# Kernel optimization log

Measured on AMD Instinct MI355X. Metric: run time of the kernel, lower is better.

The kernel has to match this reference:

```python
import jax, jax.numpy as jnp
import numpy as np

B, T, NX = 2, 2048, 512
H = 2                    # n_head (structurally forced to 2 by rns() broadcasting)
L = 64                   # num landmarks (cfg.MODEL.LANDMARK)
K = 32                   # rns neighbors per token
HD = NX // H // 2        # differential head dim = 128
EPS = 1e-5


def setup_inputs() -> dict:
    key = jax.random.key(0)
    ks = jax.random.split(key, 16)
    inp = {}
    inp["x"] = jax.random.normal(ks[0], (B, T, NX), jnp.float32)
    # linear weights (torch nn.Linear stores [out,in], applies x @ W.T)
    inp["wq"] = jax.random.normal(ks[1], (NX, NX), jnp.float32) * 0.02
    inp["wk"] = jax.random.normal(ks[2], (NX, NX), jnp.float32) * 0.02
    inp["wv"] = jax.random.normal(ks[3], (NX, NX), jnp.float32) * 0.02
    inp["wo"] = jax.random.normal(ks[4], (NX, NX), jnp.float32) * 0.02
    # landmark modulation params (kaiming-normal-ish init)
    inp["m1"] = jax.random.normal(ks[5], (2 * H, L, 1), jnp.float32)
    inp["m2"] = jax.random.normal(ks[6], (2 * H, 1, L), jnp.float32)
    # differential-attention lambda params
    inp["lq1"] = jax.random.normal(ks[7], (HD,), jnp.float32) * 0.1
    inp["lk1"] = jax.random.normal(ks[8], (HD,), jnp.float32) * 0.1
    inp["lq2"] = jax.random.normal(ks[9], (HD,), jnp.float32) * 0.1
    inp["lk2"] = jax.random.normal(ks[10], (HD,), jnp.float32) * 0.1
    inp["rms_g"] = jnp.ones((2 * HD,), jnp.float32)
    inp["l"] = 3  # layer depth for lambda_init_fn
    inp["num_landmark"] = L
    inp["rns_indices"] = jax.random.randint(ks[11], (B, T, K), 0, T)
    # random.sample(range(t), L) -> distinct indices
    inp["landmark"] = jax.random.permutation(ks[12], T)[:L]
    return inp


def _forward(x, wq, wk, wv, wo, m1, m2, lq1, lk1, lq2, lk2, rms_g,
             l, rns_indices, landmark):
    b, t, nx = x.shape
    hd = nx // H // 2
    q = x @ wq.T
    k = x @ wk.T
    v = x @ wv.T
    qh = q.reshape(b, t, 2 * H, hd).transpose(0, 2, 1, 3)   # [b,2H,t,hd]
    kh = k.reshape(b, t, 2 * H, hd).transpose(0, 2, 3, 1)   # [b,2H,hd,t]
    vh = v.reshape(b, t, H, 2 * hd).transpose(0, 2, 1, 3)   # [b,H,t,2hd]

    # landmark (Nystrom) low-rank factors, L2-normalized over head dim
    sq = qh[:, :, landmark, :]                               # [b,2H,L,hd]
    sk = kh[:, :, :, landmark]                               # [b,2H,hd,L]
    sq = sq / jnp.linalg.norm(sq, axis=3, keepdims=True)
    sk = sk / jnp.linalg.norm(sk, axis=2, keepdims=True)
    sq = m1[None] * sq
    sk = m2[None] * sk

    w1 = jnp.matmul(qh, sk)                                  # [b,2H,t,L]
    w2 = jnp.matmul(sq, kh)                                  # [b,2H,L,t]
    w = jnp.matmul(w1, w2)                                   # [b,2H,t,t]

    lam_init = 0.8 - 0.6 * np.exp(-0.3 * l)
    lam = jnp.exp(jnp.sum(lq1 * lk1)) - jnp.exp(jnp.sum(lq2 * lk2)) + lam_init

    # rns symmetric sparse mask: mask[b,i,j]=1 iff j in rns_indices[b,i] AND i in rns_indices[b,j]
    bi = jnp.arange(b)[:, None, None]
    ti = jnp.arange(t)[None, :, None]
    m = jnp.zeros((b, t, t), x.dtype).at[bi, ti, rns_indices].set(1.0)
    m = m * m.transpose(0, 2, 1)
    m4 = m[:, None]                                          # broadcast over heads

    p = jax.nn.softmax(w * m4 - 1e9 * (1.0 - m4), axis=-1)   # [b,2H,t,t]
    p5 = p.reshape(b, H, 2, t, t)
    # differential mixing (note: second term indexes the HEAD dim, requires H==2)
    wmix = (p5[:, :, 0] - lam * p5[:, :, 1]) + ((1.0 - lam) * p5[:, 1] - p5[:, 0])
    a = jnp.matmul(wmix, vh)                                 # [b,H,t,2hd]

    # RMSNorm sub-layer + (1 - lambda_init) scaling
    a = a * jax.lax.rsqrt(jnp.mean(a * a, axis=-1, keepdims=True) + EPS) * rms_g
    a = a * (1.0 - lam_init)
    return a.transpose(0, 2, 1, 3).reshape(b, t, H * 2 * hd) @ wo.T


def reference(x, wq, wk, wv, wo, m1, m2, lq1, lk1, lq2, lk2, rms_g,
              l, num_landmark, rns_indices, landmark):
    return _forward(x, wq, wk, wv, wo, m1, m2, lq1, lk1, lq2, lk2, rms_g,
                    l, rns_indices, landmark)
```

## Files before the change

kernel.cpp:

```cpp
#include <hip/hip_runtime.h>
#include <hip/hip_bf16.h>

#define BB 2
#define TT 2048
#define NX 512
#define NH 4
#define HD 128
#define LL 64
#define KK 32

typedef __bf16 bf16x8 __attribute__((ext_vector_type(8)));
typedef float f32x4 __attribute__((ext_vector_type(4)));
typedef unsigned short us;
typedef const unsigned int __attribute__((address_space(1)))* gptr_t;
typedef unsigned int __attribute__((address_space(3)))* lptr_t;

__device__ __forceinline__ us f2bf(float f) {
    unsigned u = __float_as_uint(f);
    unsigned r = (u + 0x7fffu + ((u >> 16) & 1u)) >> 16;
    return (us)r;
}
__device__ __forceinline__ float bf2f(us h) {
    return __uint_as_float(((unsigned)h) << 16);
}

__global__ void k_split_all(const float* __restrict__ x,
                            const float* __restrict__ wq, const float* __restrict__ wk,
                            const float* __restrict__ wv, const float* __restrict__ wo,
                            us* __restrict__ x_hi, us* __restrict__ x_lo,
                            us* __restrict__ wqkv_hi, us* __restrict__ wqkv_lo,
                            us* __restrict__ wo_hi, us* __restrict__ wo_lo,
                            const float* __restrict__ lq1, const float* __restrict__ lk1,
                            const float* __restrict__ lq2, const float* __restrict__ lk2,
                            const int* __restrict__ lint, float* __restrict__ scal)
{
    const int bidx = blockIdx.x;
    if (bidx == 3072) {
        const int tid = threadIdx.x;
        if (tid < 64) {
            float s1 = lq1[tid] * lk1[tid] + lq1[tid + 64] * lk1[tid + 64];
            float s2 = lq2[tid] * lk2[tid] + lq2[tid + 64] * lk2[tid + 64];
            for (int off = 32; off; off >>= 1) { s1 += __shfl_xor(s1, off); s2 += __shfl_xor(s2, off); }
            if (tid == 0) {
                float lam_init = 0.8f - 0.6f * expf(-0.3f * (float)lint[0]);
                scal[0] = expf(s1) - expf(s2) + lam_init;
                scal[1] = lam_init;
            }
        }
        return;
    }
    const float* src;
    us* hi;
    us* lo;
    int pos;
    if (bidx < 2048) {
        src = x; hi = x_hi; lo = x_lo;
        pos = bidx * 1024 + threadIdx.x * 4;
    } else {
        const int w = (bidx - 2048) >> 8;
        const int p = (bidx - 2048) & 255;
        pos = p * 1024 + threadIdx.x * 4;
        if (w == 0)      { src = wq; hi = wqkv_hi;          lo = wqkv_lo; }
        else if (w == 1) { src = wk; hi = wqkv_hi + 262144; lo = wqkv_lo + 262144; }
        else if (w == 2) { src = wv; hi = wqkv_hi + 524288; lo = wqkv_lo + 524288; }
        else             { src = wo; hi = wo_hi;            lo = wo_lo; }
    }
    const float4 v = *reinterpret_cast<const float4*>(src + pos);
    ushort4 h, l;
    h.x = f2bf(v.x); l.x = f2bf(v.x - bf2f(h.x));
    h.y = f2bf(v.y); l.y = f2bf(v.y - bf2f(h.y));
    h.z = f2bf(v.z); l.z = f2bf(v.z - bf2f(h.z));
    h.w = f2bf(v.w); l.w = f2bf(v.w - bf2f(h.w));
    *reinterpret_cast<ushort4*>(hi + pos) = h;
    *reinterpret_cast<ushort4*>(lo + pos) = l;
}

template<int BN, int MODE>
__global__ __launch_bounds__(256) void k_gemm_big(
    const us* __restrict__ a_hi, const us* __restrict__ a_lo,
    const us* __restrict__ b_hi, const us* __restrict__ b_lo,
    float* __restrict__ c2, float* __restrict__ cout,
    us* __restrict__ qs_hi, us* __restrict__ qs_lo,
    us* __restrict__ ks_hi, us* __restrict__ ks_lo)
{
    constexpr int NB = BN / 32;
    constexpr int NSTEP = (MODE == 0 ? 24 : 16);
    __shared__ us lsA[64 * 64];
    __shared__ us lsB[BN * 64];
    const int tid = threadIdx.x;
    const int m0 = blockIdx.x * 64, n0 = blockIdx.y * BN;
    const int region = n0 >> 9;
    const int ncol0 = n0 & 511;
    const int l = tid & 63, wid = tid >> 6;
    const int wr = (wid >> 1) * 32, wc = (wid & 1) * (BN / 2);
    const int lr = l & 15;
    const int lkb = (l >> 4) * 16;
    f32x4 acc[2][NB] = {};

    const int r8 = tid >> 3;
    const int swzc8 = (((tid & 7) ^ (r8 & 7)) * 8);

    for (int kt = 0; kt < NSTEP; ++kt) {
        const int seg = kt >> 3;
        const int koff = (kt & 7) * 64;
        const us* ab;
        const us* bb;
        if constexpr (MODE == 0) {
            ab = (seg < 2 ? a_hi : a_lo) + koff + swzc8;
            bb = (seg == 1 ? b_lo : b_hi) + koff + swzc8;
        } else {
            ab = (seg == 0 ? a_hi : a_lo) + koff + swzc8;
            bb = b_hi + koff + swzc8;
        }
        #pragma unroll
        for (int j = 0; j < 2; ++j)
            __builtin_amdgcn_global_load_lds((gptr_t)(ab + (size_t)(m0 + j * 32 + r8) * 512),
                                             (lptr_t)(lsA + j * 2048 + tid * 8), 16, 0, 0);
        #pragma unroll
        for (int j = 0; j < BN / 32; ++j)
            __builtin_amdgcn_global_load_lds((gptr_t)(bb + (size_t)(n0 + j * 32 + r8) * 512),
                                             (lptr_t)(lsB + j * 2048 + tid * 8), 16, 0, 0);
        __syncthreads();
        bf16x8 af[2][2], bfr[NB][2];
        #pragma unroll
        for (int m = 0; m < 2; ++m) {
            const int row = wr + m * 16 + lr;
            #pragma unroll
            for (int kk = 0; kk < 2; ++kk) {
                const int cb = (kk * 64 + lkb) ^ ((row & 7) << 4);
                af[m][kk] = *reinterpret_cast<const bf16x8*>(
                    (const char*)lsA + row * 128 + cb);
            }
        }
        #pragma unroll
        for (int n = 0; n < NB; ++n) {
            const int row = wc + n * 16 + lr;
            #pragma unroll
            for (int kk = 0; kk < 2; ++kk) {
                const int cb = (kk * 64 + lkb) ^ ((row & 7) << 4);
                bfr[n][kk] = *reinterpret_cast<const bf16x8*>(
                    (const char*)lsB + row * 128 + cb);
            }
        }
        #pragma unroll
        for (int kk = 0; kk < 2; ++kk)
            #pragma unroll
            for (int m = 0; m < 2; ++m)
                #pragma unroll
                for (int n = 0; n < NB; ++n)
                    acc[m][n] = __builtin_amdgcn_mfma_f32_16x16x32_bf16(
                        af[m][kk], bfr[n][kk], acc[m][n], 0, 0, 0);
        __syncthreads();
    }

    if constexpr (MODE == 0) {
        if (region < 2) {
            us* sh = (region == 0) ? qs_hi : ks_hi;
            us* slo = (region == 0) ? qs_lo : ks_lo;
            #pragma unroll
            for (int m = 0; m < 2; ++m) {
                const int row = m0 + wr + m * 16 + (l >> 4) * 4;
                #pragma unroll
                for (int n = 0; n < NB; ++n) {
                    const int col = ncol0 + wc + n * 16 + lr;
                    #pragma unroll
                    for (int r = 0; r < 4; ++r) {
                        const float val = acc[m][n][r];
                        const us h = f2bf(val);
                        sh[(size_t)(row + r) * 512 + col] = h;
                        slo[(size_t)(row + r) * 512 + col] = f2bf(val - bf2f(h));
                    }
                }
            }
        } else {
            #pragma unroll
            for (int m = 0; m < 2; ++m) {
                const int row = m0 + wr + m * 16 + (l >> 4) * 4;
                #pragma unroll
                for (int n = 0; n < NB; ++n) {
                    const int col = ncol0 + wc + n * 16 + lr;
                    #pragma unroll
                    for (int r = 0; r < 4; ++r)
                        c2[(size_t)(row + r) * 512 + col] = acc[m][n][r];
                }
            }
        }
    } else {
        #pragma unroll
        for (int m = 0; m < 2; ++m) {
            const int row = m0 + wr + m * 16 + (l >> 4) * 4;
            #pragma unroll
            for (int n = 0; n < NB; ++n) {
                const int col = n0 + wc + n * 16 + lr;
                #pragma unroll
                for (int r = 0; r < 4; ++r)
                    cout[(size_t)(row + r) * 512 + col] = acc[m][n][r];
            }
        }
    }
}

__global__ __launch_bounds__(256) void k_gemm_w12(
    const us* __restrict__ q_hi, const us* __restrict__ q_lo,
    const us* __restrict__ k_hi, const us* __restrict__ k_lo,
    const us* __restrict__ kn_hi, const us* __restrict__ kn_lo,
    const us* __restrict__ qn_hi, const us* __restrict__ qn_lo,
    float* __restrict__ w1, float* __restrict__ w2t)
{
    __shared__ us lsA[64 * 32];
    __shared__ us lsB[64 * 32];
    const int tid = threadIdx.x;
    const int m0 = blockIdx.x * 64;
    const int bh = blockIdx.y;
    const int h = bh & 3, b = bh >> 2;
    const int z = blockIdx.z;
    const us* ah = (z ? k_hi : q_hi) + ((size_t)b * 2048) * 512 + h * 128;
    const us* al = (z ? k_lo : q_lo) + ((size_t)b * 2048) * 512 + h * 128;
    const us* bh_p = (z ? qn_hi : kn_hi) + (size_t)bh * 64 * 128;
    const us* bl_p = (z ? qn_lo : kn_lo) + (size_t)bh * 64 * 128;
    float* C = (z ? w2t : w1) + (size_t)bh * 2048 * 64;

    const int l = tid & 63, wid = tid >> 6;
    const int wr = (wid >> 1) * 32, wc = (wid & 1) * 32;
    const int lr = l & 15, lk8 = (l >> 4) * 8;
    f32x4 acc[2][2] = {};
    const int srow = tid >> 2, scol = (tid & 3) * 8;

    for (int kt = 0; kt < 12; ++kt) {
        const int seg = kt >> 2;
        const int koff = (kt & 3) * 32;
        const us* ab = (seg < 2 ? ah : al) + koff + scol;
        const us* bb = (seg == 1 ? bl_p : bh_p) + koff + scol;
        __builtin_amdgcn_global_load_lds((gptr_t)(ab + (size_t)(m0 + srow) * 512),
                                         (lptr_t)(lsA + tid * 8), 16, 0, 0);
        __builtin_amdgcn_global_load_lds((gptr_t)(bb + (size_t)srow * 128),
                                         (lptr_t)(lsB + tid * 8), 16, 0, 0);
        __syncthreads();
        bf16x8 af[2], bfr[2];
        #pragma unroll
        for (int m = 0; m < 2; ++m)
            af[m] = *reinterpret_cast<const bf16x8*>(&lsA[(wr + m * 16 + lr) * 32 + lk8]);
        #pragma unroll
        for (int n = 0; n < 2; ++n)
            bfr[n] = *reinterpret_cast<const bf16x8*>(&lsB[(wc + n * 16 + lr) * 32 + lk8]);
        #pragma unroll
        for (int m = 0; m < 2; ++m)
            #pragma unroll
            for (int n = 0; n < 2; ++n)
                acc[m][n] = __builtin_amdgcn_mfma_f32_16x16x32_bf16(af[m], bfr[n], acc[m][n], 0, 0, 0);
        __syncthreads();
    }

    #pragma unroll
    for (int m = 0; m < 2; ++m) {
        const int row = m0 + wr + m * 16 + (l >> 4) * 4;
        #pragma unroll
        for (int n = 0; n < 2; ++n) {
            const int col = wc + n * 16 + lr;
            #pragma unroll
            for (int r = 0; r < 4; ++r)
                C[(size_t)(row + r) * 64 + col] = acc[m][n][r];
        }
    }
}

__global__ void k_norm_lm(const us* __restrict__ q_hi, const us* __restrict__ q_lo,
                          const us* __restrict__ k_hi, const us* __restrict__ k_lo,
                          const float* __restrict__ m1, const float* __restrict__ m2,
                          const int* __restrict__ landmark,
                          us* __restrict__ qn_hi, us* __restrict__ qn_lo,
                          us* __restrict__ kn_hi, us* __restrict__ kn_lo)
{
    const int idx = blockIdx.x;
    const int l = idx & 63;
    const int h = (idx >> 6) & 3;
    const int b = idx >> 8;
    const int lm = landmark[l];
    const int d = threadIdx.x;

    const size_t qoff = ((size_t)(b * TT + lm)) * NX + h * HD;
    const float qa = bf2f(q_hi[qoff + d]) + bf2f(q_lo[qoff + d]);
    const float qb = bf2f(q_hi[qoff + d + 64]) + bf2f(q_lo[qoff + d + 64]);
    const float ka = bf2f(k_hi[qoff + d]) + bf2f(k_lo[qoff + d]);
    const float kb = bf2f(k_hi[qoff + d + 64]) + bf2f(k_lo[qoff + d + 64]);
    float sq = qa * qa + qb * qb;
    float sk = ka * ka + kb * kb;
    for (int off = 32; off; off >>= 1) { sq += __shfl_xor(sq, off); sk += __shfl_xor(sk, off); }
    const float invq = rsqrtf(sq) * m1[h * LL + l];
    const float invk = rsqrtf(sk) * m2[h * LL + l];
    const size_t base = (((size_t)(b * NH + h)) * LL + l) * HD;
    const float vq0 = qa * invq, vq1 = qb * invq;
    const float vk0 = ka * invk, vk1 = kb * invk;
    us h0;
    h0 = f2bf(vq0); qn_hi[base + d] = h0;      qn_lo[base + d] = f2bf(vq0 - bf2f(h0));
    h0 = f2bf(vq1); qn_hi[base + d + 64] = h0; qn_lo[base + d + 64] = f2bf(vq1 - bf2f(h0));
    h0 = f2bf(vk0); kn_hi[base + d] = h0;      kn_lo[base + d] = f2bf(vk0 - bf2f(h0));
    h0 = f2bf(vk1); kn_hi[base + d + 64] = h0; kn_lo[base + d + 64] = f2bf(vk1 - bf2f(h0));
}

__global__ void k_colsum(const float* __restrict__ v, float* __restrict__ cs)
{
    const int e = blockIdx.x * 256 + threadIdx.x;
    const int b = e >> 9, c = e & 511;
    const int t0 = blockIdx.y * 128;
    const float* p = v + ((size_t)b) * TT * NX + c;
    float s = 0.f;
    for (int t = t0; t < t0 + 128; ++t) s += p[(size_t)t * NX];
    atomicAdd(&cs[e], s);
}

__global__ __launch_bounds__(256) void k_sparse_attn(
    const float* __restrict__ w1, const float* __restrict__ w2t,
    const float* __restrict__ v, const float* __restrict__ cs,
    const int* __restrict__ rns, const float* __restrict__ rms_g,
    const float* __restrict__ scal,
    us* __restrict__ ao_hi, us* __restrict__ ao_lo)
{
    const int wid = threadIdx.x >> 6;
    const int lane = threadIdx.x & 63;
    const int bi = blockIdx.x * 4 + wid;
    const int b = bi >> 11, i = bi & 2047;

    __shared__ int   sl[4][32];
    __shared__ float plog[4][96];
    __shared__ float wmm[4][2][32];
    __shared__ float w1s[4][3][64];

    const int myidx = lane & 31;
    const int cand = rns[(size_t)bi * KK + myidx];
    int dup = 0;
    #pragma unroll
    for (int kk = 0; kk < 31; ++kk) {
        const int other = __shfl(cand, kk);
        dup |= (kk < myidx) & (other == cand);
    }
    const int* jrow = rns + ((size_t)(b * TT + cand)) * KK + (lane >> 5) * 16;
    int found = 0;
    #pragma unroll
    for (int kk = 0; kk < 16; ++kk) found |= (jrow[kk] == i);
    found |= __shfl_xor(found, 32);
    const int keep = (!dup) && found;
    const unsigned long long mask = __ballot(keep) & 0xffffffffull;
    const int sc = __popcll(mask);
    const int pos = __popcll(mask & ((1ull << myidx) - 1ull));
    if (lane < 32 && keep) sl[wid][pos] = cand;

    const float lam = scal[0], lam_init = scal[1];

    if (sc > 0) {
        #pragma unroll
        for (int r = 0; r < 3; ++r) {
            const int t = r * 64 + lane;
            const int hh = t >> 6, l2 = t & 63;
            w1s[wid][hh][l2] = w1[(((size_t)(b * NH + hh + 1)) * TT + i) * LL + l2];
        }
        const int ntask = 3 * sc;
        for (int t0 = 0; t0 < ntask; t0 += 8) {
            const int t = t0 + (lane >> 3);
            float part = 0.f;
            if (t < ntask) {
                const int hh = t % 3, ss = t / 3;
                const int j = sl[wid][ss];
                const float* w2row = w2t + (((size_t)(b * NH + hh + 1)) * TT + j) * LL + (lane & 7) * 8;
                const float* w1p = &w1s[wid][hh][(lane & 7) * 8];
                #pragma unroll
                for (int e = 0; e < 8; ++e) part += w1p[e] * w2row[e];
            }
            part += __shfl_xor(part, 1);
            part += __shfl_xor(part, 2);
            part += __shfl_xor(part, 4);
            if (t < ntask && (lane & 7) == 0) plog[wid][t] = part;
        }
        if (lane < 3) {
            float mx = -1e30f;
            for (int ss = 0; ss < sc; ++ss) mx = fmaxf(mx, plog[wid][ss * 3 + lane]);
            float s = 0.f;
            for (int ss = 0; ss < sc; ++ss) {
                const float e = expf(plog[wid][ss * 3 + lane] - mx);
                plog[wid][ss * 3 + lane] = e;
                s += e;
            }
            const float inv = 1.0f / s;
            for (int ss = 0; ss < sc; ++ss) plog[wid][ss * 3 + lane] *= inv;
        }
        if (lane < sc) {
            const float p1 = plog[wid][lane * 3 + 0];
            const float p2 = plog[wid][lane * 3 + 1];
            const float p3 = plog[wid][lane * 3 + 2];
            wmm[wid][0][lane] = (1.0f - lam) * p2 - lam * p1;
            wmm[wid][1][lane] = p2 - p1 + (1.0f - 2.0f * lam) * p3;
        }
    }

    f32x4 acc0 = {0.f, 0.f, 0.f, 0.f}, acc1 = {0.f, 0.f, 0.f, 0.f};
    if (sc == 0) {
        const float cc = (1.0f - 2.0f * lam) * (1.0f / (float)TT);
        const f32x4 c0 = *reinterpret_cast<const f32x4*>(cs + b * NX + lane * 4);
        const f32x4 c1 = *reinterpret_cast<const f32x4*>(cs + b * NX + 256 + lane * 4);
        acc0 = cc * c0;
        acc1 = cc * c1;
    } else {
        for (int ss = 0; ss < sc; ++ss) {
            const float wa = wmm[wid][0][ss], wb = wmm[wid][1][ss];
            const float* vrow = v + ((size_t)(b * TT + sl[wid][ss])) * NX;
            const f32x4 va = *reinterpret_cast<const f32x4*>(vrow + lane * 4);
            const f32x4 vb = *reinterpret_cast<const f32x4*>(vrow + 256 + lane * 4);
            acc0 += wa * va;
            acc1 += wb * vb;
        }
    }

    float s0 = acc0[0]*acc0[0] + acc0[1]*acc0[1] + acc0[2]*acc0[2] + acc0[3]*acc0[3];
    float s1 = acc1[0]*acc1[0] + acc1[1]*acc1[1] + acc1[2]*acc1[2] + acc1[3]*acc1[3];
    #pragma unroll
    for (int off = 32; off; off >>= 1) { s0 += __shfl_xor(s0, off); s1 += __shfl_xor(s1, off); }
    const float sc0 = rsqrtf(s0 * (1.0f / 256.0f) + 1e-5f);
    const float sc1 = rsqrtf(s1 * (1.0f / 256.0f) + 1e-5f);
    const float og = 1.0f - lam_init;
    const f32x4 g = *reinterpret_cast<const f32x4*>(rms_g + lane * 4);
    ushort4 h0, l0, h1, l1;
    #pragma unroll
    for (int e = 0; e < 4; ++e) {
        const float v0 = acc0[e] * sc0 * g[e] * og;
        const float v1 = acc1[e] * sc1 * g[e] * og;
        const us a = f2bf(v0);
        const us bq = f2bf(v1);
        (&h0.x)[e] = a;  (&l0.x)[e] = f2bf(v0 - bf2f(a));
        (&h1.x)[e] = bq; (&l1.x)[e] = f2bf(v1 - bf2f(bq));
    }
    *reinterpret_cast<ushort4*>(ao_hi + (size_t)bi * NX + lane * 4) = h0;
    *reinterpret_cast<ushort4*>(ao_lo + (size_t)bi * NX + lane * 4) = l0;
    *reinterpret_cast<ushort4*>(ao_hi + (size_t)bi * NX + 256 + lane * 4) = h1;
    *reinterpret_cast<ushort4*>(ao_lo + (size_t)bi * NX + 256 + lane * 4) = l1;
}

extern "C" void kernel_launch(void* const* d_in, const int* in_sizes, int n_in,
                              void* d_out, int out_size, void* d_ws, size_t ws_size,
                              hipStream_t stream)
{
    const float* x    = (const float*)d_in[0];
    const float* wq   = (const float*)d_in[1];
    const float* wk   = (const float*)d_in[2];
    const float* wv   = (const float*)d_in[3];
    const float* wo   = (const float*)d_in[4];
    const float* m1   = (const float*)d_in[5];
    const float* m2   = (const float*)d_in[6];
    const float* lq1  = (const float*)d_in[7];
    const float* lk1  = (const float*)d_in[8];
    const float* lq2  = (const float*)d_in[9];
    const float* lk2  = (const float*)d_in[10];
    const float* rmsg = (const float*)d_in[11];
    const int*   lint = (const int*)d_in[12];
    const int*   rns  = (const int*)d_in[14];
    const int*   lmk  = (const int*)d_in[15];
    float* out = (float*)d_out;
    float* ws  = (float*)d_ws;

    const size_t M2 = 2097152;
    float* v    = ws;
    float* w1   = ws + M2;
    float* w2t  = ws + M2 + 1048576;
    float* cs   = ws + 2 * M2 + 1048576;
    float* scal = cs + 1024;
    us* S = (us*)(cs + 2048);
    us* x_hi = S;
    us* x_lo = S + M2;
    us* ao_hi = x_hi;
    us* ao_lo = x_lo;
    us* q_hi = S + 2 * M2;
    us* q_lo = S + 3 * M2;
    us* k_hi = S + 4 * M2;
    us* k_lo = S + 5 * M2;
    us* wqkv_hi = S + 6 * M2;
    us* wqkv_lo = wqkv_hi + 786432;
    us* wo_hi = wqkv_lo + 786432;
    us* wo_lo = wo_hi + 262144;
    us* qn_hi = wo_lo + 262144;
    us* qn_lo = qn_hi + 65536;
    us* kn_hi = qn_lo + 65536;
    us* kn_lo = kn_hi + 65536;

    k_split_all<<<3073, 256, 0, stream>>>(x, wq, wk, wv, wo,
                                          x_hi, x_lo, wqkv_hi, wqkv_lo, wo_hi, wo_lo,
                                          lq1, lk1, lq2, lk2, lint, scal);

    k_gemm_big<128, 0><<<dim3(64, 12), 256, 0, stream>>>(
        x_hi, x_lo, wqkv_hi, wqkv_lo, v, nullptr, q_hi, q_lo, k_hi, k_lo);

    k_norm_lm<<<512, 64, 0, stream>>>(q_hi, q_lo, k_hi, k_lo, m1, m2, lmk,
                                      qn_hi, qn_lo, kn_hi, kn_lo);
    hipMemsetAsync(cs, 0, 1024 * sizeof(float), stream);
    k_colsum<<<dim3(4, 16), 256, 0, stream>>>(v, cs);
    k_gemm_w12<<<dim3(32, 8, 2), 256, 0, stream>>>(q_hi, q_lo, k_hi, k_lo,
                                                   kn_hi, kn_lo, qn_hi, qn_lo, w1, w2t);
    k_sparse_attn<<<1024, 256, 0, stream>>>(w1, w2t, v, cs, rns, rmsg, scal, ao_hi, ao_lo);

    k_gemm_big<64, 1><<<dim3(64, 8), 256, 0, stream>>>(
        ao_hi, ao_lo, wo_hi, wo_lo, nullptr, out, nullptr, nullptr, nullptr, nullptr);
}
```

Baseline: 157.8 us.

## Store V in bf16, skip unused head 0 in W12, fold memset into split

The QKV GEMM uses fewer split-precision passes for the V region and writes V as bf16 instead of fp32. This halves V traffic for the column-sum and sparse-attention gathers. The landmark W1/W2 GEMM now computes only heads 1-3, since head 0 is never read, and the colsum zeroing moves from a separate memset into the split kernel. The risk is lower V precision, because the lo-part products are dropped and V is rounded to bf16.

```diff
diff --git a/kernel.cpp b/kernel.cpp
--- a/kernel.cpp
+++ b/kernel.cpp
@@ -32,11 +32,14 @@
                             us* __restrict__ wo_hi, us* __restrict__ wo_lo,
                             const float* __restrict__ lq1, const float* __restrict__ lk1,
                             const float* __restrict__ lq2, const float* __restrict__ lk2,
-                            const int* __restrict__ lint, float* __restrict__ scal)
+                            const int* __restrict__ lint, float* __restrict__ scal,
+                            float* __restrict__ cs)
 {
     const int bidx = blockIdx.x;
     if (bidx == 3072) {
         const int tid = threadIdx.x;
+        const f32x4 z = {0.f, 0.f, 0.f, 0.f};
+        *reinterpret_cast<f32x4*>(cs + tid * 4) = z;
         if (tid < 64) {
             float s1 = lq1[tid] * lk1[tid] + lq1[tid + 64] * lk1[tid + 64];
             float s2 = lq2[tid] * lk2[tid] + lq2[tid + 64] * lk2[tid + 64];
@@ -79,12 +82,11 @@
 __global__ __launch_bounds__(256) void k_gemm_big(
     const us* __restrict__ a_hi, const us* __restrict__ a_lo,
     const us* __restrict__ b_hi, const us* __restrict__ b_lo,
-    float* __restrict__ c2, float* __restrict__ cout,
+    us* __restrict__ vb, float* __restrict__ cout,
     us* __restrict__ qs_hi, us* __restrict__ qs_lo,
     us* __restrict__ ks_hi, us* __restrict__ ks_lo)
 {
     constexpr int NB = BN / 32;
-    constexpr int NSTEP = (MODE == 0 ? 24 : 16);
     __shared__ us lsA[64 * 64];
     __shared__ us lsB[BN * 64];
     const int tid = threadIdx.x;
@@ -100,14 +102,20 @@
     const int r8 = tid >> 3;
     const int swzc8 = (((tid & 7) ^ (r8 & 7)) * 8);
 
-    for (int kt = 0; kt < NSTEP; ++kt) {
+    const int nstep = (MODE == 0) ? (region < 2 ? 24 : 16) : 16;
+    for (int kt = 0; kt < nstep; ++kt) {
         const int seg = kt >> 3;
         const int koff = (kt & 7) * 64;
         const us* ab;
         const us* bb;
         if constexpr (MODE == 0) {
-            ab = (seg < 2 ? a_hi : a_lo) + koff + swzc8;
-            bb = (seg == 1 ? b_lo : b_hi) + koff + swzc8;
+            if (region < 2) {
+                ab = (seg < 2 ? a_hi : a_lo) + koff + swzc8;
+                bb = (seg == 1 ? b_lo : b_hi) + koff + swzc8;
+            } else {
+                ab = (seg == 0 ? a_hi : a_lo) + koff + swzc8;
+                bb = b_hi + koff + swzc8;
+            }
         } else {
             ab = (seg == 0 ? a_hi : a_lo) + koff + swzc8;
             bb = b_hi + koff + swzc8;
@@ -181,7 +189,7 @@
                     const int col = ncol0 + wc + n * 16 + lr;
                     #pragma unroll
                     for (int r = 0; r < 4; ++r)
-                        c2[(size_t)(row + r) * 512 + col] = acc[m][n][r];
+                        vb[(size_t)(row + r) * 512 + col] = f2bf(acc[m][n][r]);
                 }
             }
         }
@@ -211,14 +219,15 @@
     __shared__ us lsB[64 * 32];
     const int tid = threadIdx.x;
     const int m0 = blockIdx.x * 64;
-    const int bh = blockIdx.y;
-    const int h = bh & 3, b = bh >> 2;
+    const int y = blockIdx.y;
+    const int hh = y % 3, b = y / 3;
+    const int h = hh + 1;
     const int z = blockIdx.z;
     const us* ah = (z ? k_hi : q_hi) + ((size_t)b * 2048) * 512 + h * 128;
     const us* al = (z ? k_lo : q_lo) + ((size_t)b * 2048) * 512 + h * 128;
-    const us* bh_p = (z ? qn_hi : kn_hi) + (size_t)bh * 64 * 128;
-    const us* bl_p = (z ? qn_lo : kn_lo) + (size_t)bh * 64 * 128;
-    float* C = (z ? w2t : w1) + (size_t)bh * 2048 * 64;
+    const us* bh_p = (z ? qn_hi : kn_hi) + (size_t)(b * 4 + h) * 64 * 128;
+    const us* bl_p = (z ? qn_lo : kn_lo) + (size_t)(b * 4 + h) * 64 * 128;
+    float* C = (z ? w2t : w1) + (size_t)(b * 3 + hh) * 2048 * 64;
 
     const int l = tid & 63, wid = tid >> 6;
     const int wr = (wid >> 1) * 32, wc = (wid & 1) * 32;
@@ -298,20 +307,27 @@
     h0 = f2bf(vk1); kn_hi[base + d + 64] = h0; kn_lo[base + d + 64] = f2bf(vk1 - bf2f(h0));
 }
 
-__global__ void k_colsum(const float* __restrict__ v, float* __restrict__ cs)
-{
-    const int e = blockIdx.x * 256 + threadIdx.x;
-    const int b = e >> 9, c = e & 511;
-    const int t0 = blockIdx.y * 128;
-    const float* p = v + ((size_t)b) * TT * NX + c;
-    float s = 0.f;
-    for (int t = t0; t < t0 + 128; ++t) s += p[(size_t)t * NX];
-    atomicAdd(&cs[e], s);
+__global__ void k_colsum(const us* __restrict__ vb, float* __restrict__ cs)
+{
+    const int tid = threadIdx.x;
+    const int c4 = tid * 4;
+    const int b = c4 >> 9, c = c4 & 511;
+    const int t0 = blockIdx.x * 64;
+    const us* p = vb + ((size_t)(b * TT + t0)) * NX + c;
+    f32x4 s = {0.f, 0.f, 0.f, 0.f};
+    for (int t = 0; t < 64; ++t) {
+        const ushort4 u = *reinterpret_cast<const ushort4*>(p + (size_t)t * NX);
+        s[0] += bf2f(u.x); s[1] += bf2f(u.y); s[2] += bf2f(u.z); s[3] += bf2f(u.w);
+    }
+    atomicAdd(&cs[c4 + 0], s[0]);
+    atomicAdd(&cs[c4 + 1], s[1]);
+    atomicAdd(&cs[c4 + 2], s[2]);
+    atomicAdd(&cs[c4 + 3], s[3]);
 }
 
 __global__ __launch_bounds__(256) void k_sparse_attn(
     const float* __restrict__ w1, const float* __restrict__ w2t,
-    const float* __restrict__ v, const float* __restrict__ cs,
+    const us* __restrict__ vb, const float* __restrict__ cs,
     const int* __restrict__ rns, const float* __restrict__ rms_g,
     const float* __restrict__ scal,
     us* __restrict__ ao_hi, us* __restrict__ ao_lo)
@@ -352,7 +368,7 @@
         for (int r = 0; r < 3; ++r) {
             const int t = r * 64 + lane;
             const int hh = t >> 6, l2 = t & 63;
-            w1s[wid][hh][l2] = w1[(((size_t)(b * NH + hh + 1)) * TT + i) * LL + l2];
+            w1s[wid][hh][l2] = w1[(((size_t)(b * 3 + hh)) * TT + i) * LL + l2];
         }
         const int ntask = 3 * sc;
         for (int t0 = 0; t0 < ntask; t0 += 8) {
@@ -361,7 +377,7 @@
             if (t < ntask) {
                 const int hh = t % 3, ss = t / 3;
                 const int j = sl[wid][ss];
-                const float* w2row = w2t + (((size_t)(b * NH + hh + 1)) * TT + j) * LL + (lane & 7) * 8;
+                const float* w2row = w2t + (((size_t)(b * 3 + hh)) * TT + j) * LL + (lane & 7) * 8;
                 const float* w1p = &w1s[wid][hh][(lane & 7) * 8];
                 #pragma unroll
                 for (int e = 0; e < 8; ++e) part += w1p[e] * w2row[e];
@@ -402,11 +418,13 @@
     } else {
         for (int ss = 0; ss < sc; ++ss) {
             const float wa = wmm[wid][0][ss], wb = wmm[wid][1][ss];
-            const float* vrow = v + ((size_t)(b * TT + sl[wid][ss])) * NX;
-            const f32x4 va = *reinterpret_cast<const f32x4*>(vrow + lane * 4);
-            const f32x4 vb = *reinterpret_cast<const f32x4*>(vrow + 256 + lane * 4);
-            acc0 += wa * va;
-            acc1 += wb * vb;
+            const us* vrow = vb + ((size_t)(b * TT + sl[wid][ss])) * NX;
+            const ushort4 ua = *reinterpret_cast<const ushort4*>(vrow + lane * 4);
+            const ushort4 ub = *reinterpret_cast<const ushort4*>(vrow + 256 + lane * 4);
+            acc0[0] += wa * bf2f(ua.x); acc0[1] += wa * bf2f(ua.y);
+            acc0[2] += wa * bf2f(ua.z); acc0[3] += wa * bf2f(ua.w);
+            acc1[0] += wb * bf2f(ub.x); acc1[1] += wb * bf2f(ub.y);
+            acc1[2] += wb * bf2f(ub.z); acc1[3] += wb * bf2f(ub.w);
         }
     }
 
@@ -457,21 +475,22 @@
     float* ws  = (float*)d_ws;
 
     const size_t M2 = 2097152;
-    float* v    = ws;
-    float* w1   = ws + M2;
-    float* w2t  = ws + M2 + 1048576;
-    float* cs   = ws + 2 * M2 + 1048576;
+    const size_t W3 = 786432;
+    float* w1   = ws;
+    float* w2t  = ws + W3;
+    float* cs   = ws + 2 * W3;
     float* scal = cs + 1024;
-    us* S = (us*)(cs + 2048);
-    us* x_hi = S;
-    us* x_lo = S + M2;
+    us* S = (us*)(scal + 128);
+    us* vb   = S;
+    us* x_hi = S + M2;
+    us* x_lo = S + 2 * M2;
     us* ao_hi = x_hi;
     us* ao_lo = x_lo;
-    us* q_hi = S + 2 * M2;
-    us* q_lo = S + 3 * M2;
-    us* k_hi = S + 4 * M2;
-    us* k_lo = S + 5 * M2;
-    us* wqkv_hi = S + 6 * M2;
+    us* q_hi = S + 3 * M2;
+    us* q_lo = S + 4 * M2;
+    us* k_hi = S + 5 * M2;
+    us* k_lo = S + 6 * M2;
+    us* wqkv_hi = S + 7 * M2;
     us* wqkv_lo = wqkv_hi + 786432;
     us* wo_hi = wqkv_lo + 786432;
     us* wo_lo = wo_hi + 262144;
@@ -482,18 +501,17 @@
 
     k_split_all<<<3073, 256, 0, stream>>>(x, wq, wk, wv, wo,
                                           x_hi, x_lo, wqkv_hi, wqkv_lo, wo_hi, wo_lo,
-                                          lq1, lk1, lq2, lk2, lint, scal);
+                                          lq1, lk1, lq2, lk2, lint, scal, cs);
 
     k_gemm_big<128, 0><<<dim3(64, 12), 256, 0, stream>>>(
-        x_hi, x_lo, wqkv_hi, wqkv_lo, v, nullptr, q_hi, q_lo, k_hi, k_lo);
+        x_hi, x_lo, wqkv_hi, wqkv_lo, vb, nullptr, q_hi, q_lo, k_hi, k_lo);
 
     k_norm_lm<<<512, 64, 0, stream>>>(q_hi, q_lo, k_hi, k_lo, m1, m2, lmk,
                                       qn_hi, qn_lo, kn_hi, kn_lo);
-    hipMemsetAsync(cs, 0, 1024 * sizeof(float), stream);
-    k_colsum<<<dim3(4, 16), 256, 0, stream>>>(v, cs);
-    k_gemm_w12<<<dim3(32, 8, 2), 256, 0, stream>>>(q_hi, q_lo, k_hi, k_lo,
+    k_colsum<<<32, 256, 0, stream>>>(vb, cs);
+    k_gemm_w12<<<dim3(32, 6, 2), 256, 0, stream>>>(q_hi, q_lo, k_hi, k_lo,
                                                    kn_hi, kn_lo, qn_hi, qn_lo, w1, w2t);
-    k_sparse_attn<<<1024, 256, 0, stream>>>(w1, w2t, v, cs, rns, rmsg, scal, ao_hi, ao_lo);
+    k_sparse_attn<<<1024, 256, 0, stream>>>(w1, w2t, vb, cs, rns, rmsg, scal, ao_hi, ao_lo);
 
     k_gemm_big<64, 1><<<dim3(64, 8), 256, 0, stream>>>(
         ao_hi, ao_lo, wo_hi, wo_lo, nullptr, out, nullptr, nullptr, nullptr, nullptr);
```

Result: faster. 150.4 us (-4.7%).
